# Kernel tuning notes

Hardware: AMD Instinct MI355X
Metric: run time of the kernel (lower is better)

The kernel has to match this reference:

```python
import jax, jax.numpy as jnp
import numpy as np

B, S, H = 256, 512, 256  # batch, seq_len, input_size == hidden_size (forced by h_shape logic)


def setup_inputs() -> dict:
    key = jax.random.key(0)
    ks = jax.random.split(key, 8)
    scale = 1.0 / np.sqrt(H)

    def w(k, shape):
        return jax.random.normal(k, shape, dtype=jnp.float32) * scale

    # x last feature channel doubles as the (nonnegative) time-delta signal
    x = jax.random.uniform(ks[0], (B, S, H), dtype=jnp.float32)
    return dict(
        x=x,
        Wx0=w(ks[1], (H, 4 * H)), Wh0=w(ks[2], (H, 4 * H)), b0=jnp.zeros((4 * H,), jnp.float32),
        Wd0=w(ks[3], (H, H)), bd0=jnp.zeros((H,), jnp.float32),
        Wx1=w(ks[4], (H, 4 * H)), Wh1=w(ks[5], (H, 4 * H)), b1=jnp.zeros((4 * H,), jnp.float32),
        Wd1=w(ks[6], (H, H)), bd1=jnp.zeros((H,), jnp.float32),
    )


def _tlstm_layer(x, Wx, Wh, b, Wd, bd):
    """One T-LSTM layer over a full sequence. x: [B, S, F] -> ([B, S, H], hT, cT)."""
    # Precompute input projections for all timesteps (hoisted out of the recurrence)
    xg = jnp.einsum('bsf,fg->bsg', x, Wx) + b          # [B, S, 4H]
    dt = x[..., -1:]                                    # time delta channel [B, S, 1]
    decay = 1.0 / jnp.log(jnp.e + dt)                   # 'log' time-decay g(dt)

    h0 = jnp.zeros((x.shape[0], Wh.shape[0]), x.dtype)
    c0 = jnp.zeros_like(h0)

    def step(carry, inp):
        h, c = carry
        xg_t, dec_t = inp
        # T-LSTM memory decomposition: decay short-term component of cell state
        cs = jnp.tanh(c @ Wd + bd)                      # short-term memory C_S
        c_adj = c - cs + cs * dec_t                     # C_T + C_S * g(dt)
        g = xg_t + h @ Wh                               # fused gate pre-activations [B, 4H]
        i, f, o, cand = jnp.split(g, 4, axis=-1)
        c_new = jax.nn.sigmoid(f) * c_adj + jax.nn.sigmoid(i) * jnp.tanh(cand)
        h_new = jax.nn.sigmoid(o) * jnp.tanh(c_new)
        return (h_new, c_new), h_new

    (hT, cT), hs = jax.lax.scan(
        step, (h0, c0), (jnp.swapaxes(xg, 0, 1), jnp.swapaxes(decay, 0, 1)))
    return jnp.swapaxes(hs, 0, 1), hT, cT               # [B, S, H], [B, H], [B, H]


def reference(x, Wx0, Wh0, b0, Wd0, bd0, Wx1, Wh1, b1, Wd1, bd1):
    y0, h0, c0 = _tlstm_layer(x, Wx0, Wh0, b0, Wd0, bd0)
    y1, h1, c1 = _tlstm_layer(y0, Wx1, Wh1, b1, Wd1, bd1)
    # matches (layer_output, last_state_list) of the torch module, flattened
    return (y1, h0, c0, h1, c1)
```

## Files before the change

### kernel.cpp

```cpp
#include <hip/hip_runtime.h>
#include <stdint.h>

#define B_ 256
#define S_ 512
#define H_ 256
#define G_ 1024
#define CHUNK 32
#define NCHUNK (S_ / CHUNK)

typedef __attribute__((ext_vector_type(8))) short bf16x8;
typedef __attribute__((ext_vector_type(4))) float f32x4;

__device__ __forceinline__ unsigned short f2bf(float f) {
    unsigned u = __builtin_bit_cast(unsigned, f);
    unsigned r = u + 0x7fffu + ((u >> 16) & 1u);
    return (unsigned short)(r >> 16);
}
__device__ __forceinline__ float bf2f(unsigned short v) {
    return __builtin_bit_cast(float, (unsigned)v << 16);
}
__device__ __forceinline__ float bfbits_lo(unsigned v) {
    return __builtin_bit_cast(float, (unsigned)(v << 16));
}
__device__ __forceinline__ float bfbits_hi(unsigned v) {
    return __builtin_bit_cast(float, v & 0xffff0000u);
}
__device__ __forceinline__ float sigmoidf_(float x) { return 1.f / (1.f + __expf(-x)); }
__device__ __forceinline__ float tanhf_(float x) { return 2.f / (1.f + __expf(-2.f * x)) - 1.f; }

__global__ void prep_w(const float* __restrict__ W, unsigned short* __restrict__ Wp, int NT) {
    int tid = blockIdx.x * 256 + threadIdx.x;
    int total = NT * 8 * 64;
    if (tid >= total) return;
    int l = tid & 63, kk = (tid >> 6) & 7, nt = tid >> 9;
    int n = nt * 16 + (l & 15);
    int k0 = kk * 32 + (l >> 4) * 8;
    int N = NT * 16;
    unsigned short v[8];
#pragma unroll
    for (int i = 0; i < 8; i++) v[i] = f2bf(W[(size_t)(k0 + i) * N + n]);
    uint4 o;
    o.x = (unsigned)v[0] | ((unsigned)v[1] << 16);
    o.y = (unsigned)v[2] | ((unsigned)v[3] << 16);
    o.z = (unsigned)v[4] | ((unsigned)v[5] << 16);
    o.w = (unsigned)v[6] | ((unsigned)v[7] << 16);
    *(uint4*)(Wp + (size_t)tid * 8) = o;
}

__global__ void prep_decay(const float* __restrict__ x, float* __restrict__ dec, int n) {
    int i = blockIdx.x * 256 + threadIdx.x;
    if (i < n) dec[i] = 1.f / __logf(2.718281828459045f + x[(size_t)i * H_ + (H_ - 1)]);
}

template <bool SRCF32>
__device__ void gemm_body(const void* __restrict__ src, const unsigned short* __restrict__ Wp,
                          const float* __restrict__ bias, unsigned short* __restrict__ xgp,
                          int chunk, short* Albs) {
    const int tid = threadIdx.x;
    const int bx = blockIdx.x;
    const int by = blockIdx.y;
    const int r0 = bx * 128;
    const int t_loc = r0 >> 8;
    const int b0 = r0 & 255;
    const int sg = chunk * CHUNK + t_loc;
    {
        const int m = tid >> 1, kh = tid & 1;
        const size_t rowbase = ((size_t)(b0 + m) * S_ + sg) * H_ + kh * 128;
        if constexpr (SRCF32) {
            const float* p = (const float*)src + rowbase;
#pragma unroll
            for (int jo = 0; jo < 16; jo++) {
                int k = kh * 128 + jo * 8;
                float4 a = *(const float4*)(p + jo * 8);
                float4 b = *(const float4*)(p + jo * 8 + 4);
                int slot = ((m >> 4) * 8 + (k >> 5)) * 64 + ((m & 15) | (((k >> 3) & 3) << 4));
                uint4 o;
                o.x = (unsigned)f2bf(a.x) | ((unsigned)f2bf(a.y) << 16);
                o.y = (unsigned)f2bf(a.z) | ((unsigned)f2bf(a.w) << 16);
                o.z = (unsigned)f2bf(b.x) | ((unsigned)f2bf(b.y) << 16);
                o.w = (unsigned)f2bf(b.z) | ((unsigned)f2bf(b.w) << 16);
                *(uint4*)&Albs[slot * 8] = o;
            }
        } else {
            const unsigned short* p = (const unsigned short*)src + rowbase;
#pragma unroll
            for (int jo = 0; jo < 16; jo++) {
                int k = kh * 128 + jo * 8;
                uint4 o = *(const uint4*)(p + jo * 8);
                int slot = ((m >> 4) * 8 + (k >> 5)) * 64 + ((m & 15) | (((k >> 3) & 3) << 4));
                *(uint4*)&Albs[slot * 8] = o;
            }
        }
    }
    __syncthreads();
    const int w = tid >> 6, l = tid & 63;
    const int wm = w >> 1, wn = w & 1;
    const int col = l & 15;
    float bv[4];
#pragma unroll
    for (int q = 0; q < 4; q++) bv[q] = bias[(by * 8 + wn * 4 + q) * 16 + col];
    f32x4 acc[4][4];
#pragma unroll
    for (int mi = 0; mi < 4; mi++)
#pragma unroll
        for (int q = 0; q < 4; q++) {
            acc[mi][q][0] = bv[q]; acc[mi][q][1] = bv[q];
            acc[mi][q][2] = bv[q]; acc[mi][q][3] = bv[q];
        }
    const bf16x8* Wp8 = (const bf16x8*)Wp;
#pragma unroll
    for (int kk = 0; kk < 8; kk++) {
        bf16x8 af[4], bfr[4];
#pragma unroll
        for (int mi = 0; mi < 4; mi++)
            af[mi] = *(const bf16x8*)&Albs[(((wm * 4 + mi) * 8 + kk) * 64 + l) * 8];
#pragma unroll
        for (int q = 0; q < 4; q++)
            bfr[q] = Wp8[((size_t)(by * 8 + wn * 4 + q) * 8 + kk) * 64 + l];
#pragma unroll
        for (int mi = 0; mi < 4; mi++)
#pragma unroll
            for (int q = 0; q < 4; q++)
                acc[mi][q] = __builtin_amdgcn_mfma_f32_16x16x32_bf16(af[mi], bfr[q], acc[mi][q], 0, 0, 0);
    }
    const int rblk0 = r0 >> 4;
#pragma unroll
    for (int mi = 0; mi < 4; mi++) {
        int rowblk = rblk0 + wm * 4 + mi;
#pragma unroll
        for (int q = 0; q < 4; q++) {
            int qg = by * 8 + wn * 4 + q;
            uint2 o;
            o.x = (unsigned)f2bf(acc[mi][q][0]) | ((unsigned)f2bf(acc[mi][q][1]) << 16);
            o.y = (unsigned)f2bf(acc[mi][q][2]) | ((unsigned)f2bf(acc[mi][q][3]) << 16);
            *(uint2*)&xgp[(((size_t)rowblk * 64 + qg) * 64 + l) * 4] = o;
        }
    }
}

__global__ __launch_bounds__(256) void gemm_dual(const float* __restrict__ x,
                                                 const unsigned short* __restrict__ y0bf,
                                                 const unsigned short* __restrict__ Wp0,
                                                 const float* __restrict__ bias0,
                                                 const unsigned short* __restrict__ Wp1,
                                                 const float* __restrict__ bias1,
                                                 unsigned short* __restrict__ xgpA,
                                                 unsigned short* __restrict__ xgpB, int c0, int c1) {
    extern __shared__ short Albs[];
    if (blockIdx.z == 0) {
        if (c0 < 0) return;
        gemm_body<true>(x, Wp0, bias0, xgpA, c0, Albs);
    } else {
        if (c1 < 0) return;
        gemm_body<false>(y0bf, Wp1, bias1, xgpB, c1, Albs);
    }
}

template <bool ISL0>
__device__ void rec_run(const unsigned short* __restrict__ xgp, const bf16x8* __restrict__ Whp8,
                        const bf16x8* __restrict__ Wdp8, const float* __restrict__ bd,
                        const float* __restrict__ dec_in, void* __restrict__ yout,
                        float* __restrict__ dec_out, unsigned short* __restrict__ h_state,
                        float* __restrict__ c_state, int chunk, int bblk, char* smem) {
    const int tid = threadIdx.x;
    const int w = tid >> 6, l = tid & 63;
    const int lgrp = l >> 4, col = l & 15;
    const int b0 = bblk * 16;
    const int n = w * 16 + col;
    const float bdv = bd[n];

    bf16x8 wd[8];
#pragma unroll
    for (int kk = 0; kk < 8; kk++) wd[kk] = Wdp8[((size_t)w * 8 + kk) * 64 + l];

    float creg[4];
    {
        short* hb0 = (short*)smem;
        short* cb0 = (short*)(smem + 8192);
        if (chunk == 0) {
#pragma unroll
            for (int r = 0; r < 4; r++) creg[r] = 0.f;
            for (int i = tid; i < 4096; i += 1024) { hb0[i] = 0; cb0[i] = 0; }
        } else {
#pragma unroll
            for (int i = 0; i < 4; i++) {
                int idx = tid + i * 1024;
                int row = idx >> 8, nn = idx & 255;
                int sw = nn ^ ((row & 7) << 3);
                hb0[row * 256 + sw] = (short)h_state[(size_t)(b0 + row) * H_ + nn];
                cb0[row * 256 + sw] = (short)f2bf(c_state[(size_t)(b0 + row) * H_ + nn]);
            }
#pragma unroll
            for (int r = 0; r < 4; r++)
                creg[r] = c_state[(size_t)(b0 + lgrp * 4 + r) * H_ + n];
        }
    }
    const uint2* xg8 = (const uint2*)xgp;
    uint2 xc[4], xn[4];
#pragma unroll
    for (int q = 0; q < 4; q++)
        xc[q] = xg8[((size_t)bblk * 64 + (q * 16 + w)) * 64 + l];
    float dn[4];
#pragma unroll
    for (int r = 0; r < 4; r++)
        dn[r] = dec_in[(size_t)(b0 + lgrp * 4 + r) * S_ + chunk * CHUNK];
    __syncthreads();

    bf16x8 wfb[2][4];
#pragma unroll
    for (int q = 0; q < 4; q++) wfb[0][q] = Whp8[((size_t)(q * 16 + w) * 8 + 0) * 64 + l];
#pragma unroll
    for (int q = 0; q < 4; q++) wfb[1][q] = Whp8[((size_t)(q * 16 + w) * 8 + 1) * 64 + l];

#pragma unroll 1
    for (int t = 0; t < CHUNK; ++t) {
        const int tg = chunk * CHUNK + t;
        const int par = t & 1;
        const short* hb = (const short*)(smem + par * 16384);
        const short* cb = (const short*)(smem + par * 16384 + 8192);
        short* hx = (short*)(smem + (par ^ 1) * 16384);
        short* cx = (short*)(smem + (par ^ 1) * 16384 + 8192);
        const bf16x8* WhpT;
        {
            unsigned long long tz = 0;
            asm volatile("" : "+s"(tz));
            WhpT = (const bf16x8*)((const char*)Whp8 + tz);
        }
        float dcur[4];
#pragma unroll
        for (int r = 0; r < 4; r++) dcur[r] = dn[r];
        f32x4 csacc = {0.f, 0.f, 0.f, 0.f};
        f32x4 gacc[4];
#pragma unroll
        for (int q = 0; q < 4; q++) {
            uint2 v = xc[q];
            gacc[q][0] = bfbits_lo(v.x);
            gacc[q][1] = bfbits_hi(v.x);
            gacc[q][2] = bfbits_lo(v.y);
            gacc[q][3] = bfbits_hi(v.y);
        }
#pragma unroll
        for (int kk = 0; kk < 8; kk++) {
            const int cur = kk & 1;
            const int ha = col * 256 + ((kk * 32 + lgrp * 8) ^ ((col & 7) << 3));
            bf16x8 hf = *(const bf16x8*)&hb[ha];
            bf16x8 cf = *(const bf16x8*)&cb[ha];
            csacc = __builtin_amdgcn_mfma_f32_16x16x32_bf16(cf, wd[kk], csacc, 0, 0, 0);
#pragma unroll
            for (int q = 0; q < 4; q++)
                gacc[q] = __builtin_amdgcn_mfma_f32_16x16x32_bf16(hf, wfb[cur][q], gacc[q], 0, 0, 0);
            const int kn2 = (kk + 2) & 7;
#pragma unroll
            for (int q = 0; q < 4; q++)
                wfb[cur][q] = WhpT[((size_t)(q * 16 + w) * 8 + kn2) * 64 + l];
        }
        const int tn = (t + 1 < CHUNK) ? t + 1 : t;
        {
            int rb = tn * 16 + bblk;
#pragma unroll
            for (int q = 0; q < 4; q++)
                xn[q] = xg8[((size_t)rb * 64 + (q * 16 + w)) * 64 + l];
            int tgn = chunk * CHUNK + tn;
#pragma unroll
            for (int r = 0; r < 4; r++)
                dn[r] = dec_in[(size_t)(b0 + lgrp * 4 + r) * S_ + tgn];
        }
#pragma unroll
        for (int r = 0; r < 4; r++) {
            int row = lgrp * 4 + r;
            float cs = tanhf_(csacc[r] + bdv);
            float cadj = creg[r] - cs + cs * dcur[r];
            float iv = sigmoidf_(gacc[0][r]);
            float fv = sigmoidf_(gacc[1][r]);
            float ov = sigmoidf_(gacc[2][r]);
            float cd = tanhf_(gacc[3][r]);
            float cn = fv * cadj + iv * cd;
            float hn = ov * tanhf_(cn);
            creg[r] = cn;
            int sw = n ^ ((row & 7) << 3);
            unsigned hc;
            asm("v_cvt_pk_bf16_f32 %0, %1, %2" : "=v"(hc) : "v"(hn), "v"(cn));
            unsigned short hnb = (unsigned short)hc;
            hx[row * 256 + sw] = (short)hnb;
            cx[row * 256 + sw] = (short)(hc >> 16);
            size_t yi = ((size_t)(b0 + row) * S_ + tg) * H_ + n;
            if constexpr (ISL0) {
                ((unsigned short*)yout)[yi] = hnb;
                if (w == 15 && col == 15)
                    dec_out[(size_t)(b0 + row) * S_ + tg] = 1.f / __logf(2.718281828459045f + hn);
            } else {
                ((float*)yout)[yi] = hn;
            }
            if (t == CHUNK - 1) {
                h_state[(size_t)(b0 + row) * H_ + n] = hnb;
                c_state[(size_t)(b0 + row) * H_ + n] = cn;
            }
        }
        asm volatile("s_waitcnt lgkmcnt(0)" ::: "memory");
        __builtin_amdgcn_s_barrier();
        __builtin_amdgcn_sched_barrier(0);
#pragma unroll
        for (int q = 0; q < 4; q++) xc[q] = xn[q];
    }
}

__global__ __launch_bounds__(1024, 4) void rec_fused(
    const unsigned short* __restrict__ xgpA, const unsigned short* __restrict__ Whp0,
    const unsigned short* __restrict__ Wdp0, const float* __restrict__ bd0,
    const float* __restrict__ dec0, unsigned short* __restrict__ y0bf,
    float* __restrict__ dec1, unsigned short* __restrict__ hs0, float* __restrict__ cs0,
    const unsigned short* __restrict__ xgpB, const unsigned short* __restrict__ Whp1,
    const unsigned short* __restrict__ Wdp1, const float* __restrict__ bd1,
    float* __restrict__ y1, unsigned short* __restrict__ hs1, float* __restrict__ cs1,
    int c0, int c1) {
    extern __shared__ char smem[];
    int lay = blockIdx.x >> 4, bblk = blockIdx.x & 15;
    if (lay == 0) {
        if (c0 < 0) return;
        rec_run<true>(xgpA, (const bf16x8*)Whp0, (const bf16x8*)Wdp0, bd0, dec0, y0bf, dec1,
                      hs0, cs0, c0, bblk, smem);
    } else {
        if (c1 < 0) return;
        rec_run<false>(xgpB, (const bf16x8*)Whp1, (const bf16x8*)Wdp1, bd1, dec1, y1, nullptr,
                       hs1, cs1, c1, bblk, smem);
    }
}

__global__ void copy_tail(const unsigned short* __restrict__ h0, const float* __restrict__ c0,
                          const unsigned short* __restrict__ h1, const float* __restrict__ c1,
                          float* __restrict__ out) {
    int i = blockIdx.x * 256 + threadIdx.x;
    if (i >= 4 * 65536) return;
    int which = i >> 16, j = i & 65535;
    float v = which == 0 ? bf2f(h0[j]) : which == 1 ? c0[j] : which == 2 ? bf2f(h1[j]) : c1[j];
    out[i] = v;
}

extern "C" void kernel_launch(void* const* d_in, const int* in_sizes, int n_in, void* d_out,
                              int out_size, void* d_ws, size_t ws_size, hipStream_t stream) {
    (void)in_sizes; (void)n_in; (void)out_size; (void)ws_size;
    const float* x   = (const float*)d_in[0];
    const float* Wx0 = (const float*)d_in[1];
    const float* Wh0 = (const float*)d_in[2];
    const float* b0  = (const float*)d_in[3];
    const float* Wd0 = (const float*)d_in[4];
    const float* bd0 = (const float*)d_in[5];
    const float* Wx1 = (const float*)d_in[6];
    const float* Wh1 = (const float*)d_in[7];
    const float* b1  = (const float*)d_in[8];
    const float* Wd1 = (const float*)d_in[9];
    const float* bd1 = (const float*)d_in[10];

    char* ws = (char*)d_ws;
    size_t off = 0;
    auto take = [&](size_t bytes) { void* p = ws + off; off += (bytes + 255) & ~(size_t)255; return p; };
    unsigned short* wxp0 = (unsigned short*)take(524288);
    unsigned short* whp0 = (unsigned short*)take(524288);
    unsigned short* wdp0 = (unsigned short*)take(131072);
    unsigned short* wxp1 = (unsigned short*)take(524288);
    unsigned short* whp1 = (unsigned short*)take(524288);
    unsigned short* wdp1 = (unsigned short*)take(131072);
    float* dec0 = (float*)take(524288);
    float* dec1 = (float*)take(524288);
    unsigned short* hs0 = (unsigned short*)take(131072);
    float* cs0 = (float*)take(262144);
    unsigned short* hs1 = (unsigned short*)take(131072);
    float* cs1 = (float*)take(262144);
    unsigned short* y0bf = (unsigned short*)take(67108864);
    unsigned short* xgpA = (unsigned short*)take(16777216);
    unsigned short* xgpB = (unsigned short*)take(16777216);

    const size_t smem_rec = 32768;
    (void)hipFuncSetAttribute(reinterpret_cast<const void*>(&rec_fused),
                              hipFuncAttributeMaxDynamicSharedMemorySize, (int)smem_rec);
    (void)hipFuncSetAttribute(reinterpret_cast<const void*>(&gemm_dual),
                              hipFuncAttributeMaxDynamicSharedMemorySize, 65536);

    prep_w<<<128, 256, 0, stream>>>(Wx0, wxp0, 64);
    prep_w<<<128, 256, 0, stream>>>(Wh0, whp0, 64);
    prep_w<<<32, 256, 0, stream>>>(Wd0, wdp0, 16);
    prep_w<<<128, 256, 0, stream>>>(Wx1, wxp1, 64);
    prep_w<<<128, 256, 0, stream>>>(Wh1, whp1, 64);
    prep_w<<<32, 256, 0, stream>>>(Wd1, wdp1, 16);
    prep_decay<<<512, 256, 0, stream>>>(x, dec0, B_ * S_);

    float* y1 = (float*)d_out;
    for (int s = 0; s <= NCHUNK; ++s) {
        int c0 = (s < NCHUNK) ? s : -1;
        int c1 = (s >= 1) ? s - 1 : -1;
        gemm_dual<<<dim3(64, 8, 2), 256, 65536, stream>>>(x, y0bf, wxp0, b0, wxp1, b1,
                                                          xgpA, xgpB, c0, c1);
        rec_fused<<<32, 1024, smem_rec, stream>>>(xgpA, whp0, wdp0, bd0, dec0, y0bf, dec1,
                                                  hs0, cs0, xgpB, whp1, wdp1, bd1, y1,
                                                  hs1, cs1, c0, c1);
    }
    copy_tail<<<1024, 256, 0, stream>>>(hs0, cs0, hs1, cs1, y1 + (size_t)B_ * S_ * H_);
}
```

Baseline: 4.908 ms.

## Halve recurrent block size so each wave computes two hidden column tiles

The recurrent kernel now launches 512 threads per block instead of 1024, and each wave handles two 16-column hidden tiles. Each LDS h/c fragment read therefore feeds twice as many MFMAs, and the per-step barrier spans fewer waves. Wd is no longer kept resident in registers; it is streamed with double buffering alongside Wh. In exchange, per-thread register pressure roughly doubles for the accumulators and weight buffers, and fewer waves are available to hide latency.

```diff
diff --git a/kernel.cpp b/kernel.cpp
--- a/kernel.cpp
+++ b/kernel.cpp
@@ -166,51 +166,59 @@
     const int w = tid >> 6, l = tid & 63;
     const int lgrp = l >> 4, col = l & 15;
     const int b0 = bblk * 16;
-    const int n = w * 16 + col;
-    const float bdv = bd[n];
-
-    bf16x8 wd[8];
-#pragma unroll
-    for (int kk = 0; kk < 8; kk++) wd[kk] = Wdp8[((size_t)w * 8 + kk) * 64 + l];
-
-    float creg[4];
+    const int ct0 = 2 * w, ct1 = 2 * w + 1;
+    const int n0 = ct0 * 16 + col, n1 = ct1 * 16 + col;
+    const float bdv[2] = {bd[n0], bd[n1]};
+
+    float creg[2][4];
     {
         short* hb0 = (short*)smem;
         short* cb0 = (short*)(smem + 8192);
         if (chunk == 0) {
 #pragma unroll
-            for (int r = 0; r < 4; r++) creg[r] = 0.f;
-            for (int i = tid; i < 4096; i += 1024) { hb0[i] = 0; cb0[i] = 0; }
+            for (int j = 0; j < 2; j++)
+#pragma unroll
+                for (int r = 0; r < 4; r++) creg[j][r] = 0.f;
+            for (int i = tid; i < 4096; i += 512) { hb0[i] = 0; cb0[i] = 0; }
         } else {
 #pragma unroll
-            for (int i = 0; i < 4; i++) {
-                int idx = tid + i * 1024;
+            for (int i = 0; i < 8; i++) {
+                int idx = tid + i * 512;
                 int row = idx >> 8, nn = idx & 255;
                 int sw = nn ^ ((row & 7) << 3);
                 hb0[row * 256 + sw] = (short)h_state[(size_t)(b0 + row) * H_ + nn];
                 cb0[row * 256 + sw] = (short)f2bf(c_state[(size_t)(b0 + row) * H_ + nn]);
             }
 #pragma unroll
-            for (int r = 0; r < 4; r++)
-                creg[r] = c_state[(size_t)(b0 + lgrp * 4 + r) * H_ + n];
+            for (int j = 0; j < 2; j++)
+#pragma unroll
+                for (int r = 0; r < 4; r++)
+                    creg[j][r] = c_state[(size_t)(b0 + lgrp * 4 + r) * H_ + (j ? n1 : n0)];
         }
     }
     const uint2* xg8 = (const uint2*)xgp;
-    uint2 xc[4], xn[4];
-#pragma unroll
-    for (int q = 0; q < 4; q++)
-        xc[q] = xg8[((size_t)bblk * 64 + (q * 16 + w)) * 64 + l];
+    uint2 xc[2][4], xn[2][4];
+#pragma unroll
+    for (int j = 0; j < 2; j++)
+#pragma unroll
+        for (int q = 0; q < 4; q++)
+            xc[j][q] = xg8[((size_t)bblk * 64 + (q * 16 + 2 * w + j)) * 64 + l];
     float dn[4];
 #pragma unroll
     for (int r = 0; r < 4; r++)
         dn[r] = dec_in[(size_t)(b0 + lgrp * 4 + r) * S_ + chunk * CHUNK];
     __syncthreads();
 
-    bf16x8 wfb[2][4];
-#pragma unroll
-    for (int q = 0; q < 4; q++) wfb[0][q] = Whp8[((size_t)(q * 16 + w) * 8 + 0) * 64 + l];
-#pragma unroll
-    for (int q = 0; q < 4; q++) wfb[1][q] = Whp8[((size_t)(q * 16 + w) * 8 + 1) * 64 + l];
+    bf16x8 wfb[2][8], wdb[2][2];
+#pragma unroll
+    for (int p = 0; p < 2; p++)
+#pragma unroll
+        for (int j = 0; j < 2; j++) {
+#pragma unroll
+            for (int q = 0; q < 4; q++)
+                wfb[p][j * 4 + q] = Whp8[((size_t)(q * 16 + 2 * w + j) * 8 + p) * 64 + l];
+            wdb[p][j] = Wdp8[((size_t)(2 * w + j) * 8 + p) * 64 + l];
+        }
 
 #pragma unroll 1
     for (int t = 0; t < CHUNK; ++t) {
@@ -220,24 +228,29 @@
         const short* cb = (const short*)(smem + par * 16384 + 8192);
         short* hx = (short*)(smem + (par ^ 1) * 16384);
         short* cx = (short*)(smem + (par ^ 1) * 16384 + 8192);
-        const bf16x8* WhpT;
+        const bf16x8 *WhpT, *WdpT;
         {
             unsigned long long tz = 0;
             asm volatile("" : "+s"(tz));
             WhpT = (const bf16x8*)((const char*)Whp8 + tz);
+            WdpT = (const bf16x8*)((const char*)Wdp8 + tz);
         }
         float dcur[4];
 #pragma unroll
         for (int r = 0; r < 4; r++) dcur[r] = dn[r];
-        f32x4 csacc = {0.f, 0.f, 0.f, 0.f};
-        f32x4 gacc[4];
-#pragma unroll
-        for (int q = 0; q < 4; q++) {
-            uint2 v = xc[q];
-            gacc[q][0] = bfbits_lo(v.x);
-            gacc[q][1] = bfbits_hi(v.x);
-            gacc[q][2] = bfbits_lo(v.y);
-            gacc[q][3] = bfbits_hi(v.y);
+        f32x4 csacc[2];
+        f32x4 gacc[2][4];
+#pragma unroll
+        for (int j = 0; j < 2; j++) {
+            csacc[j][0] = 0.f; csacc[j][1] = 0.f; csacc[j][2] = 0.f; csacc[j][3] = 0.f;
+#pragma unroll
+            for (int q = 0; q < 4; q++) {
+                uint2 v = xc[j][q];
+                gacc[j][q][0] = bfbits_lo(v.x);
+                gacc[j][q][1] = bfbits_hi(v.x);
+                gacc[j][q][2] = bfbits_lo(v.y);
+                gacc[j][q][3] = bfbits_hi(v.y);
+            }
         }
 #pragma unroll
         for (int kk = 0; kk < 8; kk++) {
@@ -245,66 +258,83 @@
             const int ha = col * 256 + ((kk * 32 + lgrp * 8) ^ ((col & 7) << 3));
             bf16x8 hf = *(const bf16x8*)&hb[ha];
             bf16x8 cf = *(const bf16x8*)&cb[ha];
-            csacc = __builtin_amdgcn_mfma_f32_16x16x32_bf16(cf, wd[kk], csacc, 0, 0, 0);
-#pragma unroll
-            for (int q = 0; q < 4; q++)
-                gacc[q] = __builtin_amdgcn_mfma_f32_16x16x32_bf16(hf, wfb[cur][q], gacc[q], 0, 0, 0);
+#pragma unroll
+            for (int j = 0; j < 2; j++) {
+                csacc[j] = __builtin_amdgcn_mfma_f32_16x16x32_bf16(cf, wdb[cur][j], csacc[j], 0, 0, 0);
+#pragma unroll
+                for (int q = 0; q < 4; q++)
+                    gacc[j][q] = __builtin_amdgcn_mfma_f32_16x16x32_bf16(hf, wfb[cur][j * 4 + q],
+                                                                         gacc[j][q], 0, 0, 0);
+            }
             const int kn2 = (kk + 2) & 7;
 #pragma unroll
-            for (int q = 0; q < 4; q++)
-                wfb[cur][q] = WhpT[((size_t)(q * 16 + w) * 8 + kn2) * 64 + l];
+            for (int j = 0; j < 2; j++) {
+#pragma unroll
+                for (int q = 0; q < 4; q++)
+                    wfb[cur][j * 4 + q] = WhpT[((size_t)(q * 16 + 2 * w + j) * 8 + kn2) * 64 + l];
+                wdb[cur][j] = WdpT[((size_t)(2 * w + j) * 8 + kn2) * 64 + l];
+            }
         }
         const int tn = (t + 1 < CHUNK) ? t + 1 : t;
         {
             int rb = tn * 16 + bblk;
 #pragma unroll
-            for (int q = 0; q < 4; q++)
-                xn[q] = xg8[((size_t)rb * 64 + (q * 16 + w)) * 64 + l];
+            for (int j = 0; j < 2; j++)
+#pragma unroll
+                for (int q = 0; q < 4; q++)
+                    xn[j][q] = xg8[((size_t)rb * 64 + (q * 16 + 2 * w + j)) * 64 + l];
             int tgn = chunk * CHUNK + tn;
 #pragma unroll
             for (int r = 0; r < 4; r++)
                 dn[r] = dec_in[(size_t)(b0 + lgrp * 4 + r) * S_ + tgn];
         }
 #pragma unroll
-        for (int r = 0; r < 4; r++) {
-            int row = lgrp * 4 + r;
-            float cs = tanhf_(csacc[r] + bdv);
-            float cadj = creg[r] - cs + cs * dcur[r];
-            float iv = sigmoidf_(gacc[0][r]);
-            float fv = sigmoidf_(gacc[1][r]);
-            float ov = sigmoidf_(gacc[2][r]);
-            float cd = tanhf_(gacc[3][r]);
-            float cn = fv * cadj + iv * cd;
-            float hn = ov * tanhf_(cn);
-            creg[r] = cn;
-            int sw = n ^ ((row & 7) << 3);
-            unsigned hc;
-            asm("v_cvt_pk_bf16_f32 %0, %1, %2" : "=v"(hc) : "v"(hn), "v"(cn));
-            unsigned short hnb = (unsigned short)hc;
-            hx[row * 256 + sw] = (short)hnb;
-            cx[row * 256 + sw] = (short)(hc >> 16);
-            size_t yi = ((size_t)(b0 + row) * S_ + tg) * H_ + n;
-            if constexpr (ISL0) {
-                ((unsigned short*)yout)[yi] = hnb;
-                if (w == 15 && col == 15)
-                    dec_out[(size_t)(b0 + row) * S_ + tg] = 1.f / __logf(2.718281828459045f + hn);
-            } else {
-                ((float*)yout)[yi] = hn;
-            }
-            if (t == CHUNK - 1) {
-                h_state[(size_t)(b0 + row) * H_ + n] = hnb;
-                c_state[(size_t)(b0 + row) * H_ + n] = cn;
+        for (int j = 0; j < 2; j++) {
+            const int n = j ? n1 : n0;
+#pragma unroll
+            for (int r = 0; r < 4; r++) {
+                int row = lgrp * 4 + r;
+                float cs = tanhf_(csacc[j][r] + bdv[j]);
+                float cadj = creg[j][r] - cs + cs * dcur[r];
+                float iv = sigmoidf_(gacc[j][0][r]);
+                float fv = sigmoidf_(gacc[j][1][r]);
+                float ov = sigmoidf_(gacc[j][2][r]);
+                float cd = tanhf_(gacc[j][3][r]);
+                float cn = fv * cadj + iv * cd;
+                float hn = ov * tanhf_(cn);
+                creg[j][r] = cn;
+                int sw = n ^ ((row & 7) << 3);
+                unsigned hc;
+                asm("v_cvt_pk_bf16_f32 %0, %1, %2" : "=v"(hc) : "v"(hn), "v"(cn));
+                unsigned short hnb = (unsigned short)hc;
+                hx[row * 256 + sw] = (short)hnb;
+                cx[row * 256 + sw] = (short)(hc >> 16);
+                size_t yi = ((size_t)(b0 + row) * S_ + tg) * H_ + n;
+                if constexpr (ISL0) {
+                    ((unsigned short*)yout)[yi] = hnb;
+                    if (w == 7 && j == 1 && col == 15)
+                        dec_out[(size_t)(b0 + row) * S_ + tg] =
+                            1.f / __logf(2.718281828459045f + hn);
+                } else {
+                    ((float*)yout)[yi] = hn;
+                }
+                if (t == CHUNK - 1) {
+                    h_state[(size_t)(b0 + row) * H_ + n] = hnb;
+                    c_state[(size_t)(b0 + row) * H_ + n] = cn;
+                }
             }
         }
         asm volatile("s_waitcnt lgkmcnt(0)" ::: "memory");
         __builtin_amdgcn_s_barrier();
         __builtin_amdgcn_sched_barrier(0);
 #pragma unroll
-        for (int q = 0; q < 4; q++) xc[q] = xn[q];
-    }
-}
-
-__global__ __launch_bounds__(1024, 4) void rec_fused(
+        for (int j = 0; j < 2; j++)
+#pragma unroll
+            for (int q = 0; q < 4; q++) xc[j][q] = xn[j][q];
+    }
+}
+
+__global__ __launch_bounds__(512, 2) void rec_fused(
     const unsigned short* __restrict__ xgpA, const unsigned short* __restrict__ Whp0,
     const unsigned short* __restrict__ Wdp0, const float* __restrict__ bd0,
     const float* __restrict__ dec0, unsigned short* __restrict__ y0bf,
@@ -390,9 +420,9 @@
         int c1 = (s >= 1) ? s - 1 : -1;
         gemm_dual<<<dim3(64, 8, 2), 256, 65536, stream>>>(x, y0bf, wxp0, b0, wxp1, b1,
                                                           xgpA, xgpB, c0, c1);
-        rec_fused<<<32, 1024, smem_rec, stream>>>(xgpA, whp0, wdp0, bd0, dec0, y0bf, dec1,
-                                                  hs0, cs0, xgpB, whp1, wdp1, bd1, y1,
-                                                  hs1, cs1, c0, c1);
+        rec_fused<<<32, 512, smem_rec, stream>>>(xgpA, whp0, wdp0, bd0, dec0, y0bf, dec1,
+                                                 hs0, cs0, xgpB, whp1, wdp1, bd1, y1,
+                                                 hs1, cs1, c0, c1);
     }
     copy_tail<<<1024, 256, 0, stream>>>(hs0, cs0, hs1, cs1, y1 + (size_t)B_ * S_ * H_);
 }
```

Result: slower. 5.593 ms (+14.0%).
